# Performance work log

Measured on AMD Instinct MI355X. Metric: run time of the kernel, lower is better.

## Reference

```python
import jax, jax.numpy as jnp
import numpy as np
import math

R, C, E, H = 512, 512, 256, 8
D = E // H

def setup_inputs() -> dict:
    key = jax.random.key(0)
    ks = jax.random.split(key, 10)
    x = jax.random.normal(ks[0], (R, C, E), dtype=jnp.float32)
    mask = (jax.random.uniform(ks[1], (R, C)) < 0.1).astype(jnp.float32)
    s = 1.0 / math.sqrt(E)
    Wq = jax.random.normal(ks[2], (E, E), dtype=jnp.float32) * s
    Wk = jax.random.normal(ks[3], (E, E), dtype=jnp.float32) * s
    Wv = jax.random.normal(ks[4], (E, E), dtype=jnp.float32) * s
    Wo = jax.random.normal(ks[5], (E, E), dtype=jnp.float32) * s
    bq = jnp.zeros((E,), jnp.float32)
    bk = jnp.zeros((E,), jnp.float32)
    bv = jnp.zeros((E,), jnp.float32)
    bo = jnp.zeros((E,), jnp.float32)
    return {"x": x, "mask": mask, "Wq": Wq, "bq": bq, "Wk": Wk, "bk": bk,
            "Wv": Wv, "bv": bv, "Wo": Wo, "bo": bo}

def reference(x, mask, Wq, bq, Wk, bk, Wv, bv, Wo, bo):
    r, c, e = x.shape
    scaling = (D ** -0.5) / math.sqrt(r)  # align_scaling
    # projections -> [R, C, H, D]
    q = (x @ Wq + bq).reshape(r, c, H, D)
    k = (x @ Wk + bk).reshape(r, c, H, D)
    q = q * scaling
    q = q * (1.0 - mask[:, :, None, None])  # zero padded query positions
    # shared row-summed attention logits: sum over rows r -> [H, C, C]
    attn_weights = jnp.einsum('rihd,rjhd->hij', q, k)
    m0 = mask[0][None, :, None]  # [1, C, 1] broadcast over heads and j
    attn_weights = attn_weights * (1.0 - m0) + m0 * (-10000.0)
    attn_probs = jax.nn.softmax(attn_weights, axis=-1)  # [H, C, C]
    # dropout rate is 0 -> identity
    v = (x @ Wv + bv).reshape(r, c, H, D)
    context = jnp.einsum('hij,rjhd->rihd', attn_probs, v).reshape(r, c, e)
    output = context @ Wo + bo
    return (output, attn_probs)
```

## Files before the change

### kernel.cpp

```cpp
#include <hip/hip_runtime.h>
#include <math.h>

#define R_ 512
#define C_ 512
#define E_ 256
#define H_ 8
#define D_ 32
#define RC_ (R_*C_)
#define RP 136

typedef __attribute__((ext_vector_type(8))) short bf16x8;
typedef __attribute__((ext_vector_type(4))) float f32x4;

__device__ __forceinline__ ushort f2bf(float f) {
    union { float f; unsigned u; } v; v.f = f;
    unsigned r = v.u + 0x7FFFu + ((v.u >> 16) & 1u);
    return (ushort)(r >> 16);
}
__device__ __forceinline__ float bf2f(ushort u) {
    union { unsigned u; float f; } v; v.u = ((unsigned)u) << 16;
    return v.f;
}

__device__ __forceinline__ void gll16(const ushort* g, ushort* l) {
#if __has_builtin(__builtin_amdgcn_global_load_lds)
    __builtin_amdgcn_global_load_lds(
        (const __attribute__((address_space(1))) unsigned*)(unsigned long long)g,
        (__attribute__((address_space(3))) unsigned*)(unsigned)(unsigned long long)l,
        16, 0, 0);
#else
    *(uint4*)l = *(const uint4*)g;
#endif
}

#define SCH(gbase, stride, lds, f)                                               \
    gll16((gbase) + (size_t)((f) >> 2) * (stride)                                \
              + (((((f) & 3) ^ ((((f) >> 2) >> 1) & 3))) << 3),                  \
          (lds) + (f) * 8)

#define SCHED0   __builtin_amdgcn_sched_barrier(0)
#define ABAR     __builtin_amdgcn_s_barrier()
#define VMCNT(N) asm volatile("s_waitcnt vmcnt(" #N ")" ::: "memory")

#define PREAMBLE(WM, WN)                                \
    const int t = threadIdx.x;                          \
    const int wid = t >> 6, l = t & 63;                 \
    const int wm = (WM), wn = (WN);                     \
    const int l15 = l & 15, lhi = l >> 4;               \
    const int swz8 = (lhi ^ ((l15 >> 1) & 3)) * 8;      \
    f32x4 acc[4][4];                                    \
    _Pragma("unroll")                                   \
    for (int a_ = 0; a_ < 4; ++a_)                      \
        _Pragma("unroll")                               \
        for (int b_ = 0; b_ < 4; ++b_)                  \
            acc[a_][b_] = (f32x4){0.f, 0.f, 0.f, 0.f};

#define MFMA_STEP(As, Bs)                                                        \
    {                                                                            \
        bf16x8 af_[4], bf_[4];                                                   \
        _Pragma("unroll")                                                        \
        for (int f_ = 0; f_ < 4; ++f_) {                                         \
            af_[f_] = *(const bf16x8*)((As) + (wm*64 + f_*16 + l15)*32 + swz8);  \
            bf_[f_] = *(const bf16x8*)((Bs) + (wn*64 + f_*16 + l15)*32 + swz8);  \
        }                                                                        \
        _Pragma("unroll")                                                        \
        for (int m_ = 0; m_ < 4; ++m_)                                           \
            _Pragma("unroll")                                                    \
            for (int n_ = 0; n_ < 4; ++n_)                                       \
                acc[m_][n_] = __builtin_amdgcn_mfma_f32_16x16x32_bf16(           \
                    af_[m_], bf_[n_], acc[m_][n_], 0, 0, 0);                     \
    }

#define DBUFT(STG, NIT)                                                          \
    STG(0, A0, B0); STG(1, A1, B1);                                              \
    _Pragma("unroll")                                                            \
    for (int s = 0; s < (NIT); ++s) {                                            \
        if (s < (NIT) - 1) { VMCNT(4); } else { VMCNT(0); }                      \
        SCHED0; ABAR; SCHED0;                                                    \
        if (s + 2 < (NIT)) {                                                     \
            if (((s + 2) % 3) == 0)      { STG(s + 2, A0, B0); }                 \
            else if (((s + 2) % 3) == 1) { STG(s + 2, A1, B1); }                 \
            else                         { STG(s + 2, A2, B2); }                 \
        }                                                                        \
        if ((s % 3) == 0)      { MFMA_STEP(A0, B0); }                            \
        else if ((s % 3) == 1) { MFMA_STEP(A1, B1); }                            \
        else                   { MFMA_STEP(A2, B2); }                            \
    }

#define BUFS3 ushort* A0 = S;          ushort* B0 = S + 4096;                    \
              ushort* A1 = S + 8192;   ushort* B1 = S + 12288;                   \
              ushort* A2 = S + 16384;  ushort* B2 = S + 20480;

__global__ __launch_bounds__(256) void convert_x(
    const float* __restrict__ x, ushort* __restrict__ xb)
{
    const size_t blk = (size_t)blockIdx.x * 4096;
    #pragma unroll
    for (int c = 0; c < 4; ++c) {
        const size_t s = blk + ((size_t)threadIdx.x + 256 * c) * 4;
        float4 a = *(const float4*)(x + s);
        ushort o[4] = {f2bf(a.x), f2bf(a.y), f2bf(a.z), f2bf(a.w)};
        *(uint2*)(xb + s) = *(uint2*)o;
    }
}

__global__ __launch_bounds__(256) void convert_w(
    const float* __restrict__ Wq, const float* __restrict__ Wk,
    const float* __restrict__ Wv, const float* __restrict__ Wo,
    ushort* __restrict__ WTqkv, ushort* __restrict__ WoT)
{
    const int id = blockIdx.x;
    const int matn = id >> 8;
    const int n = id & 255;
    const int k = threadIdx.x;
    const float* W = (matn == 0) ? Wq : (matn == 1) ? Wk : (matn == 2) ? Wv : Wo;
    ushort v = f2bf(W[(size_t)k * E_ + n]);
    if (matn < 3) WTqkv[((size_t)matn * E_ + n) * E_ + k] = v;
    else          WoT[(size_t)n * E_ + k] = v;
}

__global__ __launch_bounds__(256) void qkv_mfma(
    const ushort* __restrict__ xb, const ushort* __restrict__ WT,
    const float* __restrict__ bq, const float* __restrict__ bk,
    const float* __restrict__ bv, const float* __restrict__ mask,
    ushort* __restrict__ qb, ushort* __restrict__ kb, ushort* __restrict__ vb)
{
    __shared__ __align__(16) ushort S[24576];
    BUFS3;
    const int id = ((blockIdx.x & 7) * 1536) + (blockIdx.x >> 3);
    const int nt = id % 6;
    const int rc0 = (id / 6) * 128;
    PREAMBLE(wid >> 1, wid & 1);

    const ushort* Ab = xb + (size_t)rc0 * E_;
    const ushort* Bb = WT + (size_t)nt * 128 * E_;

#define QSTG(i, Abuf, Bbuf) {                                   \
    const ushort* Ai = Ab + (i) * 32;                           \
    const ushort* Bi = Bb + (i) * 32;                           \
    SCH(Ai, E_, Abuf, t); SCH(Ai, E_, Abuf, t + 256);           \
    SCH(Bi, E_, Bbuf, t); SCH(Bi, E_, Bbuf, t + 256); }
    DBUFT(QSTG, 8);
    __syncthreads();

    const int proj = nt >> 1;
    const float* bias = (proj == 0) ? bq : (proj == 1) ? bk : bv;
    float bvv[4];
    #pragma unroll
    for (int fn = 0; fn < 4; ++fn)
        bvv[fn] = bias[(nt * 128 + wn * 64 + fn * 16 + l15) & 255];

    #pragma unroll
    for (int fm = 0; fm < 4; ++fm)
        #pragma unroll
        for (int fn = 0; fn < 4; ++fn)
            #pragma unroll
            for (int rg = 0; rg < 4; ++rg) {
                const int m = wm * 64 + fm * 16 + lhi * 4 + rg;
                const int n = wn * 64 + fn * 16 + l15;
                const ushort val = f2bf(acc[fm][fn][rg] + bvv[fn]);
                if (proj < 2) S[m * RP + n] = val;
                else          S[n * RP + m] = val;
            }
    __syncthreads();

    const int r = rc0 >> 9, c0 = rc0 & 511;
    if (proj < 2) {
        ushort* dst = (proj == 0) ? qb : kb;
        #pragma unroll
        for (int c = 0; c < 8; ++c) {
            const int idx = t + 256 * c;
            const int mrow = idx >> 4, ne = (idx & 15) * 8;
            uint4 w = *(const uint4*)(S + mrow * RP + ne);
            if (proj == 0) {
                const float sk = 0.0078125f * (1.0f - mask[rc0 + mrow]);
                ushort* ws = (ushort*)&w;
                #pragma unroll
                for (int jj = 0; jj < 8; ++jj) ws[jj] = f2bf(bf2f(ws[jj]) * sk);
            }
            const int e = (nt & 1) * 128 + ne, h = e >> 5, d = e & 31;
            *(uint4*)(dst + ((((size_t)h * R_ + r) * C_) + c0 + mrow) * D_ + d) = w;
        }
    } else {
        #pragma unroll
        for (int c = 0; c < 8; ++c) {
            const int idx = t + 256 * c;
            const int nrow = idx >> 4, m0 = (idx & 15) * 8;
            uint4 w = *(const uint4*)(S + nrow * RP + m0);
            const int e = (nt & 1) * 128 + nrow, h = e >> 5, d = e & 31;
            *(uint4*)(vb + (((size_t)h * R_ + r) * D_ + d) * C_ + c0 + m0) = w;
        }
    }
}

__global__ __launch_bounds__(256) void logits_mfma(
    const ushort* __restrict__ qb, const ushort* __restrict__ kb,
    float* __restrict__ partial)
{
    __shared__ __align__(16) ushort S[24576];
    BUFS3;
    const int id = ((blockIdx.x & 7) * 128) + (blockIdx.x >> 3);
    const int sub = id & 15;
    const int j0 = (sub & 3) * 128;
    const int i0 = (sub >> 2) * 128;
    const int hks = id >> 4;
    const int h = hks >> 3, ks = hks & 7;
    PREAMBLE(wid >> 1, wid & 1);

    const ushort* Ab = qb + (((size_t)h * R_ + ks * 64) * C_ + i0) * D_;
    const ushort* Bb = kb + (((size_t)h * R_ + ks * 64) * C_ + j0) * D_;

#define LSTG(i, Abuf, Bbuf) {                                   \
    const ushort* Ai = Ab + (size_t)(i) * (C_ * D_);            \
    const ushort* Bi = Bb + (size_t)(i) * (C_ * D_);            \
    SCH(Ai, D_, Abuf, t); SCH(Ai, D_, Abuf, t + 256);           \
    SCH(Bi, D_, Bbuf, t); SCH(Bi, D_, Bbuf, t + 256); }
    DBUFT(LSTG, 64);

    float* dst = partial + ((size_t)ks * H_ + h) * C_ * C_;
    #pragma unroll
    for (int fm = 0; fm < 4; ++fm)
        #pragma unroll
        for (int rg = 0; rg < 4; ++rg) {
            const int i = i0 + wm * 64 + fm * 16 + lhi * 4 + rg;
            #pragma unroll
            for (int fn = 0; fn < 4; ++fn) {
                const int j = j0 + wn * 64 + fn * 16 + l15;
                dst[(size_t)i * C_ + j] = acc[fm][fn][rg];
            }
        }
}

__global__ __launch_bounds__(256) void softmax_kernel(
    const float* __restrict__ partial, const float* __restrict__ mask,
    float* __restrict__ probs, ushort* __restrict__ Pb)
{
    const int hi = blockIdx.x;
    const int i = hi & 511;
    const int t = threadIdx.x;
    const size_t base = (size_t)hi * C_;
    const size_t stride = (size_t)H_ * C_ * C_;
    float v0 = 0.f, v1 = 0.f;
    #pragma unroll
    for (int ksp = 0; ksp < 8; ++ksp) {
        v0 += partial[ksp * stride + base + t];
        v1 += partial[ksp * stride + base + t + 256];
    }
    const float mi = mask[i];
    const float keep = 1.0f - mi;
    v0 = v0 * keep + mi * (-10000.0f);
    v1 = v1 * keep + mi * (-10000.0f);

    float m = fmaxf(v0, v1);
    #pragma unroll
    for (int off = 32; off > 0; off >>= 1) m = fmaxf(m, __shfl_xor(m, off));
    __shared__ float red[4];
    if ((t & 63) == 0) red[t >> 6] = m;
    __syncthreads();
    m = fmaxf(fmaxf(red[0], red[1]), fmaxf(red[2], red[3]));

    const float e0 = expf(v0 - m), e1 = expf(v1 - m);
    float s = e0 + e1;
    #pragma unroll
    for (int off = 32; off > 0; off >>= 1) s += __shfl_xor(s, off);
    __syncthreads();
    if ((t & 63) == 0) red[t >> 6] = s;
    __syncthreads();
    s = red[0] + red[1] + red[2] + red[3];

    const float inv = 1.0f / s;
    const float p0 = e0 * inv, p1 = e1 * inv;
    probs[base + t] = p0;
    probs[base + t + 256] = p1;
    Pb[base + t] = f2bf(p0);
    Pb[base + t + 256] = f2bf(p1);
}

__global__ __launch_bounds__(256) void context_mfma(
    const ushort* __restrict__ Pb, const ushort* __restrict__ vb,
    ushort* __restrict__ ctxb)
{
    __shared__ __align__(16) ushort S[24576];
    BUFS3;
    const int id = ((blockIdx.x & 7) * 512) + (blockIdx.x >> 3);
    const int i0 = (id & 3) * 128;
    const int n0 = ((id >> 2) & 127) * 128;
    const int h = id >> 9;
    PREAMBLE(wid >> 1, wid & 1);

    const ushort* Ab = Pb + ((size_t)h * C_ + i0) * C_;
    const ushort* Bb = vb + ((size_t)h * R_ * D_ + n0) * C_;

#define CSTG(i, Abuf, Bbuf) {                                   \
    const ushort* Ai = Ab + (i) * 32;                           \
    const ushort* Bi = Bb + (i) * 32;                           \
    SCH(Ai, C_, Abuf, t); SCH(Ai, C_, Abuf, t + 256);           \
    SCH(Bi, C_, Bbuf, t); SCH(Bi, C_, Bbuf, t + 256); }
    DBUFT(CSTG, 16);
    __syncthreads();

    #pragma unroll
    for (int fm = 0; fm < 4; ++fm)
        #pragma unroll
        for (int fn = 0; fn < 4; ++fn)
            #pragma unroll
            for (int rg = 0; rg < 4; ++rg) {
                const int m = wm * 64 + fm * 16 + lhi * 4 + rg;
                const int n = wn * 64 + fn * 16 + l15;
                S[m * RP + n] = f2bf(acc[fm][fn][rg]);
            }
    __syncthreads();

    #pragma unroll
    for (int c = 0; c < 8; ++c) {
        const int idx = t + 256 * c;
        const int mrow = idx >> 4, nl = (idx & 15) * 8;
        uint4 w = *(const uint4*)(S + mrow * RP + nl);
        const int n = n0 + nl;
        const int rr = n >> 5, d = n & 31;
        const size_t rc = (size_t)rr * C_ + i0 + mrow;
        *(uint4*)(ctxb + rc * E_ + h * D_ + d) = w;
    }
}

__global__ __launch_bounds__(256) void out_proj_mfma(
    const ushort* __restrict__ ctxb, const ushort* __restrict__ WoT,
    const float* __restrict__ bo, float* __restrict__ out)
{
    __shared__ __align__(16) ushort S[24576];
    BUFS3;
    float* Sf = (float*)S;
    const int id = ((blockIdx.x & 7) * 512) + (blockIdx.x >> 3);
    const int n0 = (id & 1) * 128;
    const int rc0 = (id >> 1) * 128;
    PREAMBLE(wid >> 1, wid & 1);

    const ushort* Ab = ctxb + (size_t)rc0 * E_;
    const ushort* Bb = WoT + (size_t)n0 * E_;

#define OSTG(i, Abuf, Bbuf) {                                   \
    const ushort* Ai = Ab + (i) * 32;                           \
    const ushort* Bi = Bb + (i) * 32;                           \
    SCH(Ai, E_, Abuf, t); SCH(Ai, E_, Abuf, t + 256);           \
    SCH(Bi, E_, Bbuf, t); SCH(Bi, E_, Bbuf, t + 256); }
    DBUFT(OSTG, 8);
    __syncthreads();

    float bvv[4];
    #pragma unroll
    for (int fn = 0; fn < 4; ++fn)
        bvv[fn] = bo[n0 + wn * 64 + fn * 16 + l15];

    #pragma unroll
    for (int p = 0; p < 2; ++p) {
        #pragma unroll
        for (int fm = 0; fm < 4; ++fm)
            #pragma unroll
            for (int fh = 0; fh < 2; ++fh) {
                const int fn = 2 * p + fh;
                #pragma unroll
                for (int rg = 0; rg < 4; ++rg) {
                    const int m = wm * 64 + fm * 16 + lhi * 4 + rg;
                    const int s = wn * 32 + fh * 16 + l15;
                    Sf[m * 68 + s] = acc[fm][fn][rg] + bvv[fn];
                }
            }
        __syncthreads();
        #pragma unroll
        for (int c = 0; c < 8; ++c) {
            const int idx = t + 256 * c;
            const int row = idx >> 4, s0 = (idx & 15) * 4;
            float4 w = *(const float4*)(Sf + row * 68 + s0);
            const int ncol = n0 + (s0 >> 5) * 64 + (2 * p + ((s0 >> 4) & 1)) * 16 + (s0 & 15);
            *(float4*)(out + ((size_t)rc0 + row) * E_ + ncol) = w;
        }
        __syncthreads();
    }
}

extern "C" void kernel_launch(void* const* d_in, const int* in_sizes, int n_in,
                              void* d_out, int out_size, void* d_ws, size_t ws_size,
                              hipStream_t stream)
{
    const float* x    = (const float*)d_in[0];
    const float* mask = (const float*)d_in[1];
    const float* Wq   = (const float*)d_in[2];
    const float* bq   = (const float*)d_in[3];
    const float* Wk   = (const float*)d_in[4];
    const float* bk   = (const float*)d_in[5];
    const float* Wv   = (const float*)d_in[6];
    const float* bv   = (const float*)d_in[7];
    const float* Wo   = (const float*)d_in[8];
    const float* bo   = (const float*)d_in[9];

    float* out   = (float*)d_out;
    float* probs = out + (size_t)RC_ * E_;

    char* ws = (char*)d_ws;
    ushort* qb      = (ushort*)(ws);
    ushort* kb      = (ushort*)(ws + 134217728ull);
    ushort* vb      = (ushort*)(ws + 268435456ull);
    ushort* ctxb    = (ushort*)(ws + 402653184ull);
    float*  partial = (float*)(ws + 536870912ull);
    ushort* Pb      = (ushort*)(ws + 603979776ull);
    ushort* WTqkv   = (ushort*)(ws + 608174080ull);
    ushort* WoT     = (ushort*)(ws + 608567296ull);
    ushort* xb      = (ushort*)(ws + 608700416ull);

    convert_x<<<16384, 256, 0, stream>>>(x, xb);
    convert_w<<<1024, 256, 0, stream>>>(Wq, Wk, Wv, Wo, WTqkv, WoT);
    qkv_mfma<<<12288, 256, 0, stream>>>(xb, WTqkv, bq, bk, bv, mask, qb, kb, vb);
    logits_mfma<<<1024, 256, 0, stream>>>(qb, kb, partial);
    softmax_kernel<<<4096, 256, 0, stream>>>(partial, mask, probs, Pb);
    context_mfma<<<4096, 256, 0, stream>>>(Pb, vb, ctxb);
    out_proj_mfma<<<4096, 256, 0, stream>>>(ctxb, WoT, bo, out);
}
```

Baseline: 626.9 us.

## Fuse fp32-to-bf16 conversion of x into the QKV projection GEMM

Removes the separate convert_x pass and has qkv_mfma load fp32 x tiles directly into LDS, packing them to bf16 with v_cvt_pk_bf16_f32 right before the MFMAs. The pipeline goes from a triple-buffered schedule to a double-buffered one with explicit lgkmcnt/barrier sync. This avoids writing and re-reading a 128MB bf16 copy of x, but each qkv block (6 per row tile) now reads fp32 x, doubling A-tile traffic, and the conversion is redone six times.

```diff
diff --git a/kernel.cpp b/kernel.cpp
--- a/kernel.cpp
+++ b/kernel.cpp
@@ -20,6 +20,11 @@
 __device__ __forceinline__ float bf2f(ushort u) {
     union { unsigned u; float f; } v; v.u = ((unsigned)u) << 16;
     return v.f;
+}
+__device__ __forceinline__ unsigned cvtpk(float lo, float hi) {
+    unsigned r;
+    asm("v_cvt_pk_bf16_f32 %0, %1, %2" : "=v"(r) : "v"(lo), "v"(hi));
+    return r;
 }
 
 __device__ __forceinline__ void gll16(const ushort* g, ushort* l) {
@@ -41,6 +46,9 @@
 #define SCHED0   __builtin_amdgcn_sched_barrier(0)
 #define ABAR     __builtin_amdgcn_s_barrier()
 #define VMCNT(N) asm volatile("s_waitcnt vmcnt(" #N ")" ::: "memory")
+#define LGKM0    asm volatile("s_waitcnt lgkmcnt(0)" ::: "memory")
+#define SYNC_IN(N) do { VMCNT(N); SCHED0; ABAR; SCHED0; } while (0)
+#define SYNC_OUT   do { LGKM0; SCHED0; ABAR; SCHED0; } while (0)
 
 #define PREAMBLE(WM, WN)                                \
     const int t = threadIdx.x;                          \
@@ -91,19 +99,6 @@
               ushort* A1 = S + 8192;   ushort* B1 = S + 12288;                   \
               ushort* A2 = S + 16384;  ushort* B2 = S + 20480;
 
-__global__ __launch_bounds__(256) void convert_x(
-    const float* __restrict__ x, ushort* __restrict__ xb)
-{
-    const size_t blk = (size_t)blockIdx.x * 4096;
-    #pragma unroll
-    for (int c = 0; c < 4; ++c) {
-        const size_t s = blk + ((size_t)threadIdx.x + 256 * c) * 4;
-        float4 a = *(const float4*)(x + s);
-        ushort o[4] = {f2bf(a.x), f2bf(a.y), f2bf(a.z), f2bf(a.w)};
-        *(uint2*)(xb + s) = *(uint2*)o;
-    }
-}
-
 __global__ __launch_bounds__(256) void convert_w(
     const float* __restrict__ Wq, const float* __restrict__ Wk,
     const float* __restrict__ Wv, const float* __restrict__ Wo,
@@ -120,28 +115,79 @@
 }
 
 __global__ __launch_bounds__(256) void qkv_mfma(
-    const ushort* __restrict__ xb, const ushort* __restrict__ WT,
+    const float* __restrict__ x, const ushort* __restrict__ WT,
     const float* __restrict__ bq, const float* __restrict__ bk,
     const float* __restrict__ bv, const float* __restrict__ mask,
     ushort* __restrict__ qb, ushort* __restrict__ kb, ushort* __restrict__ vb)
 {
     __shared__ __align__(16) ushort S[24576];
-    BUFS3;
+    float*  Af0 = (float*)S;
+    float*  Af1 = (float*)(S + 8192);
+    ushort* B0  = S + 16384;
+    ushort* B1  = S + 20480;
     const int id = ((blockIdx.x & 7) * 1536) + (blockIdx.x >> 3);
     const int nt = id % 6;
     const int rc0 = (id / 6) * 128;
-    PREAMBLE(wid >> 1, wid & 1);
-
-    const ushort* Ab = xb + (size_t)rc0 * E_;
+    const int t = threadIdx.x;
+    const int wid = t >> 6, l = t & 63;
+    const int wm = wid >> 1, wn = wid & 1;
+    const int l15 = l & 15, lhi = l >> 4;
+    const int swz8 = (lhi ^ ((l15 >> 1) & 3)) * 8;
+    const int pA   = (lhi ^ (l15 & 3)) * 8;
+    f32x4 acc[4][4];
+    #pragma unroll
+    for (int a_ = 0; a_ < 4; ++a_)
+        #pragma unroll
+        for (int b_ = 0; b_ < 4; ++b_)
+            acc[a_][b_] = (f32x4){0.f, 0.f, 0.f, 0.f};
+
+    const float*  Ab = x + (size_t)rc0 * E_;
     const ushort* Bb = WT + (size_t)nt * 128 * E_;
 
-#define QSTG(i, Abuf, Bbuf) {                                   \
-    const ushort* Ai = Ab + (i) * 32;                           \
-    const ushort* Bi = Bb + (i) * 32;                           \
-    SCH(Ai, E_, Abuf, t); SCH(Ai, E_, Abuf, t + 256);           \
+#define QSTG(i, Af, Bbuf) {                                                      \
+    _Pragma("unroll")                                                            \
+    for (int c2 = 0; c2 < 4; ++c2) {                                             \
+        const int f = t + 256 * c2;                                              \
+        const int row = f >> 3;                                                  \
+        const int cc = (f & 7) ^ ((row & 3) << 1);                               \
+        gll16((const ushort*)(Ab + (size_t)row * E_ + (i) * 32 + cc * 4),        \
+              (ushort*)((Af) + f * 4));                                          \
+    }                                                                            \
+    const ushort* Bi = Bb + (i) * 32;                                            \
     SCH(Bi, E_, Bbuf, t); SCH(Bi, E_, Bbuf, t + 256); }
-    DBUFT(QSTG, 8);
-    __syncthreads();
+
+#define QMFMA(Af, Bs) {                                                          \
+    bf16x8 af_[4], bf_[4];                                                       \
+    _Pragma("unroll")                                                            \
+    for (int f_ = 0; f_ < 4; ++f_) {                                             \
+        const float* ap_ = (Af) + (wm*64 + f_*16 + l15) * 32 + pA;               \
+        float4 xa_ = *(const float4*)ap_;                                        \
+        float4 xc_ = *(const float4*)(ap_ + 4);                                  \
+        union { unsigned u[4]; bf16x8 v; } pk_;                                  \
+        pk_.u[0] = cvtpk(xa_.x, xa_.y); pk_.u[1] = cvtpk(xa_.z, xa_.w);          \
+        pk_.u[2] = cvtpk(xc_.x, xc_.y); pk_.u[3] = cvtpk(xc_.z, xc_.w);          \
+        af_[f_] = pk_.v;                                                         \
+        bf_[f_] = *(const bf16x8*)((Bs) + (wn*64 + f_*16 + l15)*32 + swz8);      \
+    }                                                                            \
+    _Pragma("unroll")                                                            \
+    for (int m_ = 0; m_ < 4; ++m_)                                               \
+        _Pragma("unroll")                                                        \
+        for (int n_ = 0; n_ < 4; ++n_)                                           \
+            acc[m_][n_] = __builtin_amdgcn_mfma_f32_16x16x32_bf16(               \
+                af_[m_], bf_[n_], acc[m_][n_], 0, 0, 0); }
+
+    QSTG(0, Af0, B0);
+    #pragma unroll
+    for (int itp = 0; itp < 4; ++itp) {
+        QSTG(2*itp + 1, Af1, B1);
+        SYNC_IN(6);
+        QMFMA(Af0, B0);
+        SYNC_OUT;
+        if (itp < 3) { QSTG(2*itp + 2, Af0, B0); SYNC_IN(6); }
+        else         { SYNC_IN(0); }
+        QMFMA(Af1, B1);
+        SYNC_OUT;
+    }
 
     const int proj = nt >> 1;
     const float* bias = (proj == 0) ? bq : (proj == 1) ? bk : bv;
@@ -191,6 +237,8 @@
             *(uint4*)(vb + (((size_t)h * R_ + r) * D_ + d) * C_ + c0 + m0) = w;
         }
     }
+#undef QSTG
+#undef QMFMA
 }
 
 __global__ __launch_bounds__(256) void logits_mfma(
@@ -405,11 +453,9 @@
     ushort* Pb      = (ushort*)(ws + 603979776ull);
     ushort* WTqkv   = (ushort*)(ws + 608174080ull);
     ushort* WoT     = (ushort*)(ws + 608567296ull);
-    ushort* xb      = (ushort*)(ws + 608700416ull);
-
-    convert_x<<<16384, 256, 0, stream>>>(x, xb);
+
     convert_w<<<1024, 256, 0, stream>>>(Wq, Wk, Wv, Wo, WTqkv, WoT);
-    qkv_mfma<<<12288, 256, 0, stream>>>(xb, WTqkv, bq, bk, bv, mask, qb, kb, vb);
+    qkv_mfma<<<12288, 256, 0, stream>>>(x, WTqkv, bq, bk, bv, mask, qb, kb, vb);
     logits_mfma<<<1024, 256, 0, stream>>>(qb, kb, partial);
     softmax_kernel<<<4096, 256, 0, stream>>>(partial, mask, probs, Pb);
     context_mfma<<<4096, 256, 0, stream>>>(Pb, vb, ctxb);
```

Result: faster. 614.1 us (-2.0%).

## Fuse fp32-to-bf16 conversion of x into QKV GEMM A-tile staging

Applied to the files above, without the earlier changes.

Removes the standalone convert_x kernel and its bf16 copy of x. The QKV GEMM now loads fp32 x through registers, converts with packed bf16 conversion instructions, and writes A tiles into double-buffered LDS, while B keeps the async LDS load path. This avoids writing and rereading a large intermediate. In exchange, each x tile is reread in fp32 by all six n-tile blocks, and A staging now goes through registers with extra waits.

```diff
diff --git a/kernel.cpp b/kernel.cpp
--- a/kernel.cpp
+++ b/kernel.cpp
@@ -20,6 +20,11 @@
 __device__ __forceinline__ float bf2f(ushort u) {
     union { unsigned u; float f; } v; v.u = ((unsigned)u) << 16;
     return v.f;
+}
+__device__ __forceinline__ unsigned cvtpk(float lo, float hi) {
+    unsigned r;
+    asm("v_cvt_pk_bf16_f32 %0, %1, %2" : "=v"(r) : "v"(lo), "v"(hi));
+    return r;
 }
 
 __device__ __forceinline__ void gll16(const ushort* g, ushort* l) {
@@ -41,6 +46,7 @@
 #define SCHED0   __builtin_amdgcn_sched_barrier(0)
 #define ABAR     __builtin_amdgcn_s_barrier()
 #define VMCNT(N) asm volatile("s_waitcnt vmcnt(" #N ")" ::: "memory")
+#define LGKM0    asm volatile("s_waitcnt lgkmcnt(0)" ::: "memory")
 
 #define PREAMBLE(WM, WN)                                \
     const int t = threadIdx.x;                          \
@@ -91,19 +97,6 @@
               ushort* A1 = S + 8192;   ushort* B1 = S + 12288;                   \
               ushort* A2 = S + 16384;  ushort* B2 = S + 20480;
 
-__global__ __launch_bounds__(256) void convert_x(
-    const float* __restrict__ x, ushort* __restrict__ xb)
-{
-    const size_t blk = (size_t)blockIdx.x * 4096;
-    #pragma unroll
-    for (int c = 0; c < 4; ++c) {
-        const size_t s = blk + ((size_t)threadIdx.x + 256 * c) * 4;
-        float4 a = *(const float4*)(x + s);
-        ushort o[4] = {f2bf(a.x), f2bf(a.y), f2bf(a.z), f2bf(a.w)};
-        *(uint2*)(xb + s) = *(uint2*)o;
-    }
-}
-
 __global__ __launch_bounds__(256) void convert_w(
     const float* __restrict__ Wq, const float* __restrict__ Wk,
     const float* __restrict__ Wv, const float* __restrict__ Wo,
@@ -120,27 +113,89 @@
 }
 
 __global__ __launch_bounds__(256) void qkv_mfma(
-    const ushort* __restrict__ xb, const ushort* __restrict__ WT,
+    const float* __restrict__ x, const ushort* __restrict__ WT,
     const float* __restrict__ bq, const float* __restrict__ bk,
     const float* __restrict__ bv, const float* __restrict__ mask,
     ushort* __restrict__ qb, ushort* __restrict__ kb, ushort* __restrict__ vb)
 {
-    __shared__ __align__(16) ushort S[24576];
-    BUFS3;
+    __shared__ __align__(16) ushort S[20480];
+    ushort* Ab0 = S;
+    ushort* Ab1 = S + 4096;
+    ushort* Bb0 = S + 8192;
+    ushort* Bb1 = S + 12288;
+    ushort* Bb2 = S + 16384;
     const int id = ((blockIdx.x & 7) * 1536) + (blockIdx.x >> 3);
     const int nt = id % 6;
     const int rc0 = (id / 6) * 128;
-    PREAMBLE(wid >> 1, wid & 1);
-
-    const ushort* Ab = xb + (size_t)rc0 * E_;
-    const ushort* Bb = WT + (size_t)nt * 128 * E_;
-
-#define QSTG(i, Abuf, Bbuf) {                                   \
-    const ushort* Ai = Ab + (i) * 32;                           \
-    const ushort* Bi = Bb + (i) * 32;                           \
-    SCH(Ai, E_, Abuf, t); SCH(Ai, E_, Abuf, t + 256);           \
-    SCH(Bi, E_, Bbuf, t); SCH(Bi, E_, Bbuf, t + 256); }
-    DBUFT(QSTG, 8);
+    const int t = threadIdx.x;
+    const int wid = t >> 6, l = t & 63;
+    const int wm = wid >> 1, wn = wid & 1;
+    const int l15 = l & 15, lhi = l >> 4;
+    const int swz8 = (lhi ^ ((l15 >> 1) & 3)) * 8;
+    f32x4 acc[4][4];
+    #pragma unroll
+    for (int a_ = 0; a_ < 4; ++a_)
+        #pragma unroll
+        for (int b_ = 0; b_ < 4; ++b_)
+            acc[a_][b_] = (f32x4){0.f, 0.f, 0.f, 0.f};
+
+    const float*  Ag = x + (size_t)rc0 * E_;
+    const ushort* Bg = WT + (size_t)nt * 128 * E_;
+
+    const int row0 = t >> 2;
+    const int cc = (t & 3) ^ ((row0 >> 1) & 3);
+    const float* Ap0 = Ag + (size_t)row0 * E_ + cc * 8;
+    const float* Ap1 = Ag + (size_t)(row0 + 64) * E_ + cc * 8;
+    const int ws0 = row0 * 32 + (t & 3) * 8;
+    const int ws1 = (row0 + 64) * 32 + (t & 3) * 8;
+
+    float4 rA0a, rA0b, rA0c, rA0d;
+    float4 rA1a, rA1b, rA1c, rA1d;
+
+#define ALOAD0(i) { rA0a = *(const float4*)(Ap0 + (i)*32);                       \
+                    rA0b = *(const float4*)(Ap0 + (i)*32 + 4);                   \
+                    rA0c = *(const float4*)(Ap1 + (i)*32);                       \
+                    rA0d = *(const float4*)(Ap1 + (i)*32 + 4); }
+#define ALOAD1(i) { rA1a = *(const float4*)(Ap0 + (i)*32);                       \
+                    rA1b = *(const float4*)(Ap0 + (i)*32 + 4);                   \
+                    rA1c = *(const float4*)(Ap1 + (i)*32);                       \
+                    rA1d = *(const float4*)(Ap1 + (i)*32 + 4); }
+#define AWRITE0(buf) { uint4 w0_ = { cvtpk(rA0a.x,rA0a.y), cvtpk(rA0a.z,rA0a.w), \
+                                     cvtpk(rA0b.x,rA0b.y), cvtpk(rA0b.z,rA0b.w)};\
+                       uint4 w1_ = { cvtpk(rA0c.x,rA0c.y), cvtpk(rA0c.z,rA0c.w), \
+                                     cvtpk(rA0d.x,rA0d.y), cvtpk(rA0d.z,rA0d.w)};\
+                       *(uint4*)((buf) + ws0) = w0_;                             \
+                       *(uint4*)((buf) + ws1) = w1_; }
+#define AWRITE1(buf) { uint4 w0_ = { cvtpk(rA1a.x,rA1a.y), cvtpk(rA1a.z,rA1a.w), \
+                                     cvtpk(rA1b.x,rA1b.y), cvtpk(rA1b.z,rA1b.w)};\
+                       uint4 w1_ = { cvtpk(rA1c.x,rA1c.y), cvtpk(rA1c.z,rA1c.w), \
+                                     cvtpk(rA1d.x,rA1d.y), cvtpk(rA1d.z,rA1d.w)};\
+                       *(uint4*)((buf) + ws0) = w0_;                             \
+                       *(uint4*)((buf) + ws1) = w1_; }
+#define BGLL(i, buf) { const ushort* Bi_ = Bg + (i) * 32;                        \
+                       SCH(Bi_, E_, buf, t); SCH(Bi_, E_, buf, t + 256); }
+
+    ALOAD0(0); BGLL(0, Bb0);
+    ALOAD1(1); BGLL(1, Bb1);
+
+    #pragma unroll
+    for (int s = 0; s < 8; ++s) {
+        if (s < 7) { VMCNT(6); } else { VMCNT(0); }
+        SCHED0;
+        if ((s & 1) == 0) { AWRITE0((s & 1) ? Ab1 : Ab0); }
+        else              { AWRITE1((s & 1) ? Ab1 : Ab0); }
+        LGKM0; SCHED0; ABAR; SCHED0;
+        if (s + 2 < 8) {
+            if ((s & 1) == 0) { ALOAD0(s + 2); }
+            else              { ALOAD1(s + 2); }
+            if (((s + 2) % 3) == 0)      { BGLL(s + 2, Bb0); }
+            else if (((s + 2) % 3) == 1) { BGLL(s + 2, Bb1); }
+            else                         { BGLL(s + 2, Bb2); }
+        }
+        if ((s % 3) == 0)      { MFMA_STEP(((s & 1) ? Ab1 : Ab0), Bb0); }
+        else if ((s % 3) == 1) { MFMA_STEP(((s & 1) ? Ab1 : Ab0), Bb1); }
+        else                   { MFMA_STEP(((s & 1) ? Ab1 : Ab0), Bb2); }
+    }
     __syncthreads();
 
     const int proj = nt >> 1;
@@ -191,6 +246,11 @@
             *(uint4*)(vb + (((size_t)h * R_ + r) * D_ + d) * C_ + c0 + m0) = w;
         }
     }
+#undef ALOAD0
+#undef ALOAD1
+#undef AWRITE0
+#undef AWRITE1
+#undef BGLL
 }
 
 __global__ __launch_bounds__(256) void logits_mfma(
@@ -405,11 +465,9 @@
     ushort* Pb      = (ushort*)(ws + 603979776ull);
     ushort* WTqkv   = (ushort*)(ws + 608174080ull);
     ushort* WoT     = (ushort*)(ws + 608567296ull);
-    ushort* xb      = (ushort*)(ws + 608700416ull);
-
-    convert_x<<<16384, 256, 0, stream>>>(x, xb);
+
     convert_w<<<1024, 256, 0, stream>>>(Wq, Wk, Wv, Wo, WTqkv, WoT);
-    qkv_mfma<<<12288, 256, 0, stream>>>(xb, WTqkv, bq, bk, bv, mask, qb, kb, vb);
+    qkv_mfma<<<12288, 256, 0, stream>>>(x, WTqkv, bq, bk, bv, mask, qb, kb, vb);
     logits_mfma<<<1024, 256, 0, stream>>>(qb, kb, partial);
     softmax_kernel<<<4096, 256, 0, stream>>>(partial, mask, probs, Pb);
     context_mfma<<<4096, 256, 0, stream>>>(Pb, vb, ctxb);
```

New measurement: 603.5 us. -3.7%, faster.
